# Kernel tuning notes

Hardware: AMD Instinct MI355X
Metric: run time of the kernel (lower is better)

## Reference

```python
import jax, jax.numpy as jnp
import numpy as np

NUM_HEADS = 8
IN_CH = 512
SCALING = float(IN_CH // 8) ** (-0.5)  # 0.125, as in the torch module


def _conv1x1(x, w, b):
    # x: [B,C,H,W], w: [O,C], b: [O]  (1x1 conv == channel matmul)
    return jnp.einsum('bchw,oc->bohw', x, w) + b[None, :, None, None]


def setup_inputs() -> dict:
    key = jax.random.key(0)
    ks = jax.random.split(key, 9)
    B, C, H, W = 4, IN_CH, 96, 96
    q = jax.random.normal(ks[0], (B, C, H, W), jnp.float32)
    v = jax.random.normal(ks[1], (B, C, H, W), jnp.float32)
    # xavier_uniform for [C,C] 1x1 conv weights
    limit = float(np.sqrt(6.0 / (C + C)))
    Wq = jax.random.uniform(ks[2], (C, C), jnp.float32, -limit, limit)
    Wk = jax.random.uniform(ks[3], (C, C), jnp.float32, -limit, limit)
    Wv = jax.random.uniform(ks[4], (C, C), jnp.float32, -limit, limit)
    bq = jnp.zeros((C,), jnp.float32)
    bk = jnp.zeros((C,), jnp.float32)
    bv = jnp.zeros((C,), jnp.float32)
    # gamma is init to 0 in the module; use a nonzero value so the output is nontrivial
    gamma = jax.random.normal(ks[5], (1,), jnp.float32) * 0.1
    return {'q': q, 'v': v, 'Wq': Wq, 'bq': bq, 'Wk': Wk, 'bk': bk,
            'Wv': Wv, 'bv': bv, 'gamma': gamma}


def reference(q, v, Wq, bq, Wk, bk, Wv, bv, gamma):
    B, C, H, W = q.shape
    nh = NUM_HEADS
    hd = C // nh
    t = _conv1x1(q, Wq, bq) * SCALING           # proj_query
    f = _conv1x1(q, Wk, bk)                     # proj_key
    g = _conv1x1(v, Wv, bv)                     # proj_value
    t = t.reshape(B * nh, hd, H, W)
    f = f.reshape(B * nh, hd, H, W)
    g = g.reshape(B * nh, hd, H, W)
    # criss-cross affinity: row (same y, all x') and column (same x, all y'!=y)
    e_row = jnp.einsum('bdyx,bdyi->byxi', t, f)  # [Bh, H, W, W]
    e_col = jnp.einsum('bdyx,bdix->byxi', t, f)  # [Bh, H, W, H]
    # exclude the current position from the column branch (CUDA kernel skips i==y)
    diag = (jnp.arange(H)[:, None, None] == jnp.arange(H)[None, None, :])  # [H,1,H]
    e_col = jnp.where(diag, -jnp.inf, e_col)
    attn = jax.nn.softmax(jnp.concatenate([e_row, e_col], axis=-1), axis=-1)  # [Bh,H,W,W+H]
    a_row, a_col = attn[..., :W], attn[..., W:]
    out = (jnp.einsum('byxi,bdyi->bdyx', a_row, g)
           + jnp.einsum('byxi,bdix->bdyx', a_col, g))  # [Bh, hd, H, W]
    out = out.reshape(B, C, H, W)
    return gamma[0] * out + v
```

## Files before the change

### kernel.cpp

```cpp
#include <hip/hip_runtime.h>
#include <hip/hip_bf16.h>

typedef __bf16 bf16;
typedef __attribute__((ext_vector_type(8))) __bf16 bf16x8;
typedef __attribute__((ext_vector_type(4))) float floatx4;

#define B_  4
#define C_  512
#define H_  96
#define W_  96
#define HD_ 64
#define HW_ 9216
#define BH_ 32
#define SCALING_ 0.125f
#define BHS_ 589824

static constexpr size_t T_ELEMS = (size_t)BH_ * HD_ * HW_;
static constexpr size_t S_ELEMS = (size_t)BH_ * HW_;

__global__ __launch_bounds__(256) void cast_w(
    const float* __restrict__ Wq, const float* __restrict__ Wk, const float* __restrict__ Wv,
    bf16* __restrict__ Wb)
{
    const int i  = blockIdx.x * 256 + threadIdx.x;
    const int e0 = i * 4;
    const int arr = e0 >> 18;
    const int off = e0 & 262143;
    const float* W = (arr == 0) ? Wq : (arr == 1) ? Wk : Wv;
    const float4 val = *(const float4*)(W + off);
    bf16 tmp[4] __attribute__((aligned(8)));
    tmp[0] = (bf16)val.x; tmp[1] = (bf16)val.y; tmp[2] = (bf16)val.z; tmp[3] = (bf16)val.w;
    *(uint2*)(Wb + e0) = *(const uint2*)tmp;
}

__global__ __launch_bounds__(256) void cast_qv(
    const float* __restrict__ q, const float* __restrict__ v,
    bf16* __restrict__ qbT, bf16* __restrict__ vbT)
{
    const int z = blockIdx.z;
    const int s = z >> 2, b = z & 3;
    const float* sb = (s ? v : q) + (size_t)b * C_ * HW_;
    bf16*       db = (s ? vbT : qbT) + (size_t)b * HW_ * C_;
    const int p0 = blockIdx.x * 64, c0 = blockIdx.y * 64;

    __shared__ float ts[64][65];
    const int tid = threadIdx.x;

    for (int i = tid; i < 1024; i += 256) {
        const int row = i >> 4, seg = i & 15;
        const float4 val = *(const float4*)(sb + (size_t)(c0 + row) * HW_ + p0 + seg * 4);
        ts[row][seg * 4 + 0] = val.x; ts[row][seg * 4 + 1] = val.y;
        ts[row][seg * 4 + 2] = val.z; ts[row][seg * 4 + 3] = val.w;
    }
    __syncthreads();
    for (int i = tid; i < 512; i += 256) {
        const int prow = i >> 3, cseg = i & 7;
        bf16 tmp[8] __attribute__((aligned(16)));
        #pragma unroll
        for (int k = 0; k < 8; k++) tmp[k] = (bf16)ts[cseg * 8 + k][prow];
        *(uint4*)(db + (size_t)(p0 + prow) * C_ + c0 + cseg * 8) = *(const uint4*)tmp;
    }
}

__device__ __forceinline__ void stage_tile(
    const bf16* __restrict__ A, const bf16* __restrict__ Bsrc,
    int o0, int p0, int k0, int tid, bf16* As, bf16* Bs)
{
    #pragma unroll
    for (int c = tid; c < 512; c += 256) {
        const int row = c >> 2, seg = c & 3;
        const bf16* gA = A    + (size_t)(o0 + row) * C_ + k0 + seg * 8;
        const bf16* gB = Bsrc + (size_t)(p0 + row) * C_ + k0 + seg * 8;
#if __has_builtin(__builtin_amdgcn_global_load_lds)
        char* lA = (char*)As + (size_t)(c & ~63) * 16;
        char* lB = (char*)Bs + (size_t)(c & ~63) * 16;
        __builtin_amdgcn_global_load_lds((const __attribute__((address_space(1))) void*)gA,
                                         (__attribute__((address_space(3))) void*)lA, 16, 0, 0);
        __builtin_amdgcn_global_load_lds((const __attribute__((address_space(1))) void*)gB,
                                         (__attribute__((address_space(3))) void*)lB, 16, 0, 0);
#else
        *(uint4*)((char*)As + (size_t)c * 16) = *(const uint4*)gA;
        *(uint4*)((char*)Bs + (size_t)c * 16) = *(const uint4*)gB;
#endif
    }
}

__device__ __forceinline__ void compute_tile(
    const bf16* As, const bf16* Bs,
    int mrow, int ncol, int l16, int quad, floatx4 acc[4][4])
{
    bf16x8 af[4], bf_[4];
    #pragma unroll
    for (int i = 0; i < 4; i++)
        af[i] = *(const bf16x8*)&As[(mrow + i * 16 + l16) * 32 + quad * 8];
    #pragma unroll
    for (int j = 0; j < 4; j++)
        bf_[j] = *(const bf16x8*)&Bs[(ncol + j * 16 + l16) * 32 + quad * 8];
    #pragma unroll
    for (int i = 0; i < 4; i++)
        #pragma unroll
        for (int j = 0; j < 4; j++)
            acc[i][j] = __builtin_amdgcn_mfma_f32_16x16x32_bf16(af[i], bf_[j], acc[i][j], 0, 0, 0);
}

__global__ __launch_bounds__(256) void conv_mfma(
    const bf16* __restrict__ Wb,
    const float* __restrict__ bq, const float* __restrict__ bk, const float* __restrict__ bv,
    const bf16* __restrict__ qbT, const bf16* __restrict__ vbT,
    bf16* __restrict__ tR, bf16* __restrict__ fR, bf16* __restrict__ g)
{
    const int z = blockIdx.z, arr = z >> 2, b = z & 3;
    const bf16* A    = Wb + (size_t)arr * C_ * C_;
    const bf16* Bsrc = ((arr == 2) ? vbT : qbT) + (size_t)b * HW_ * C_;
    const float* bias = (arr == 0) ? bq : (arr == 1) ? bk : bv;
    const float scale = (arr == 0) ? SCALING_ : 1.0f;

    const int p0 = blockIdx.x * 128;
    const int o0 = blockIdx.y * 128;

    __shared__ __align__(16) bf16 smem[17408];
    bf16* const As0 = smem;
    bf16* const Bs0 = smem + 4096;
    bf16* const As1 = smem + 8192;
    bf16* const Bs1 = smem + 12288;

    const int tid = threadIdx.x, lane = tid & 63;
    const int wave = tid >> 6, l16 = lane & 15, quad = lane >> 4;
    const int mrow = (wave >> 1) * 64, ncol = (wave & 1) * 64;

    floatx4 acc[4][4] = {};

    stage_tile(A, Bsrc, o0, p0, 0, tid, As0, Bs0);
    __syncthreads();

    for (int k0 = 0; k0 < C_; k0 += 64) {
        if (k0 + 32 < C_) stage_tile(A, Bsrc, o0, p0, k0 + 32, tid, As1, Bs1);
        compute_tile(As0, Bs0, mrow, ncol, l16, quad, acc);
        __syncthreads();
        if (k0 + 64 < C_) stage_tile(A, Bsrc, o0, p0, k0 + 64, tid, As0, Bs0);
        compute_tile(As1, Bs1, mrow, ncol, l16, quad, acc);
        __syncthreads();
    }

    const int TS = 136;
    if (arr < 2) {
        #pragma unroll
        for (int i = 0; i < 4; i++)
            #pragma unroll
            for (int r = 0; r < 4; r++) {
                const int ol_ = mrow + i * 16 + quad * 4 + r;
                const float bi = bias[o0 + ol_];
                #pragma unroll
                for (int j = 0; j < 4; j++) {
                    const int pl = ncol + j * 16 + l16;
                    smem[pl * TS + ol_] = (bf16)((acc[i][j][r] + bi) * scale);
                }
            }
        __syncthreads();
        bf16* dst = (arr == 0) ? tR : fR;
        #pragma unroll
        for (int c = tid; c < 2048; c += 256) {
            const int pl = c >> 4, oo = c & 15;
            const int pg = p0 + pl;
            const int y = pg / 96, x = pg - y * 96;
            const int og = o0 + oo * 8;
            const int bh = b * 8 + (og >> 6), d = og & 63;
            const size_t di = (size_t)bh * BHS_ + (size_t)y * 6144 + x * 64 + d;
            *(uint4*)(dst + di) = *(const uint4*)&smem[pl * TS + oo * 8];
        }
    } else {
        #pragma unroll
        for (int i = 0; i < 4; i++)
            #pragma unroll
            for (int r = 0; r < 4; r++) {
                const int ol_ = mrow + i * 16 + quad * 4 + r;
                const float bi = bias[o0 + ol_];
                #pragma unroll
                for (int j = 0; j < 4; j++) {
                    const int pl = ncol + j * 16 + l16;
                    smem[ol_ * TS + pl] = (bf16)(acc[i][j][r] + bi);
                }
            }
        __syncthreads();
        #pragma unroll
        for (int c = tid; c < 2048; c += 256) {
            const int ol_ = c >> 4, po = c & 15;
            const size_t di = (size_t)(b * 512 + o0 + ol_) * HW_ + p0 + po * 8;
            *(uint4*)(g + di) = *(const uint4*)&smem[ol_ * TS + po * 8];
        }
    }
}

__global__ __launch_bounds__(256) void transpose_g(const bf16* __restrict__ src, bf16* __restrict__ dst)
{
    const int plane = blockIdx.y;
    const int y0 = blockIdx.x * 32;
    const bf16* s = src + (size_t)plane * HW_;
    bf16*       d = dst + (size_t)plane * HW_;

    __shared__ bf16 ts[32][100];
    const int tid = threadIdx.x;

    #pragma unroll
    for (int i = tid; i < 768; i += 256) {
        const int row = i / 24, seg = i % 24;
        *(uint2*)&ts[row][seg * 4] = *(const uint2*)(s + (size_t)(y0 + row) * W_ + seg * 4);
    }
    __syncthreads();
    #pragma unroll
    for (int i = tid; i < 768; i += 256) {
        const int x = i >> 3, yseg = i & 7;
        bf16 tmp[4] __attribute__((aligned(8)));
        #pragma unroll
        for (int k = 0; k < 4; k++) tmp[k] = ts[yseg * 4 + k][x];
        *(uint2*)(d + (size_t)x * H_ + y0 + yseg * 4) = *(const uint2*)tmp;
    }
}

__global__ __launch_bounds__(512) void attn_col(
    const bf16* __restrict__ tR, const bf16* __restrict__ fR, const bf16* __restrict__ gT,
    bf16* __restrict__ outC, float* __restrict__ mc, float* __restrict__ lc)
{
    const int x = blockIdx.x;
    const int bh = blockIdx.y;

    __shared__ __align__(16) bf16 tl[96][72];
    __shared__ __align__(16) bf16 fl[96][72];
    __shared__ __align__(16) bf16 gl[64][104];
    __shared__ __align__(16) bf16 el[96][104];

    const int tid = threadIdx.x;
    const size_t sbase = (size_t)bh * BHS_;

    for (int i = tid; i < 768; i += 512) {
        const int y = i >> 3, oct = i & 7;
        const size_t gi = sbase + (size_t)y * 6144 + (size_t)x * 64 + oct * 8;
        *(uint4*)&tl[y][oct * 8] = *(const uint4*)(tR + gi);
        *(uint4*)&fl[y][oct * 8] = *(const uint4*)(fR + gi);
    }
    const size_t gbase = sbase + (size_t)x * 96;
    for (int i = tid; i < 768; i += 512) {
        const int d = i / 12, seg = i % 12;
        *(uint4*)&gl[d][seg * 8] = *(const uint4*)(gT + gbase + (size_t)d * HW_ + seg * 8);
    }
    __syncthreads();

    const int lane = tid & 63, wave = tid >> 6;
    const int l16 = lane & 15, quad = lane >> 4;

    #pragma unroll
    for (int it = 0; it < 5; it++) {
        const int idx = wave + it * 8;
        if (idx < 36) {
            const int mt = idx / 6, nt = idx % 6;
            floatx4 a = {};
            #pragma unroll
            for (int ks = 0; ks < 2; ks++) {
                bf16x8 af = *(const bf16x8*)&tl[mt * 16 + l16][ks * 32 + quad * 8];
                bf16x8 bf_ = *(const bf16x8*)&fl[nt * 16 + l16][ks * 32 + quad * 8];
                a = __builtin_amdgcn_mfma_f32_16x16x32_bf16(af, bf_, a, 0, 0, 0);
            }
            #pragma unroll
            for (int r = 0; r < 4; r++) {
                const int row = mt * 16 + quad * 4 + r, col = nt * 16 + l16;
                el[row][col] = (row == col) ? (bf16)(-1e30f) : (bf16)a[r];
            }
        }
    }
    __syncthreads();

    if (tid < 384) {
        const int r = tid >> 2, qu = tid & 3;
        float vals[24];
        float m = -1e30f;
        #pragma unroll
        for (int k = 0; k < 3; k++) {
            bf16x8 v8 = *(const bf16x8*)&el[r][qu * 24 + k * 8];
            #pragma unroll
            for (int e = 0; e < 8; e++) { vals[k * 8 + e] = (float)v8[e]; m = fmaxf(m, vals[k * 8 + e]); }
        }
        m = fmaxf(m, __shfl_xor(m, 1));
        m = fmaxf(m, __shfl_xor(m, 2));
        float s = 0.f;
        #pragma unroll
        for (int k = 0; k < 3; k++) {
            bf16 tmp[8] __attribute__((aligned(16)));
            #pragma unroll
            for (int e = 0; e < 8; e++) {
                const float p = __expf(vals[k * 8 + e] - m);
                s += p; tmp[e] = (bf16)p;
            }
            *(uint4*)&el[r][qu * 24 + k * 8] = *(const uint4*)tmp;
        }
        s += __shfl_xor(s, 1);
        s += __shfl_xor(s, 2);
        if (qu == 0) {
            mc[(size_t)bh * HW_ + x * 96 + r] = m;
            lc[(size_t)bh * HW_ + x * 96 + r] = s;
        }
    }
    __syncthreads();

    bf16 (*ol)[72] = tl;
    #pragma unroll
    for (int it = 0; it < 3; it++) {
        const int idx = wave + it * 8;
        const int mt = idx >> 2, nt = idx & 3;
        floatx4 a = {};
        #pragma unroll
        for (int ks = 0; ks < 3; ks++) {
            bf16x8 pf = *(const bf16x8*)&el[mt * 16 + l16][ks * 32 + quad * 8];
            bf16x8 gf = *(const bf16x8*)&gl[nt * 16 + l16][ks * 32 + quad * 8];
            a = __builtin_amdgcn_mfma_f32_16x16x32_bf16(pf, gf, a, 0, 0, 0);
        }
        #pragma unroll
        for (int r = 0; r < 4; r++)
            ol[mt * 16 + quad * 4 + r][nt * 16 + l16] = (bf16)a[r];
    }
    __syncthreads();

    bf16* ob = outC + sbase + (size_t)x * 6144;
    for (int i = tid; i < 768; i += 512) {
        const int j = i >> 3, oct = i & 7;
        *(uint4*)(ob + (size_t)j * 64 + oct * 8) = *(const uint4*)&ol[j][oct * 8];
    }
}

__global__ __launch_bounds__(512) void attn_row_merge(
    const bf16* __restrict__ tR, const bf16* __restrict__ fR, const bf16* __restrict__ g,
    const bf16* __restrict__ outC, const float* __restrict__ mc, const float* __restrict__ lc,
    const float* __restrict__ v, const float* __restrict__ gamma, float* __restrict__ out)
{
    const int y = blockIdx.x;
    const int bh = blockIdx.y;

    __shared__ __align__(16) bf16 tl[96][72];
    __shared__ __align__(16) bf16 fl[96][72];
    __shared__ __align__(16) bf16 gl[64][104];
    __shared__ __align__(16) bf16 el[96][104];
    __shared__ float mll[96], lll[96], wrl[96], wcl[96];

    const int tid = threadIdx.x;
    const size_t sbase = (size_t)bh * BHS_;
    const size_t slice = sbase + (size_t)y * 6144;

    for (int i = tid; i < 768; i += 512) {
        const int j = i >> 3, oct = i & 7;
        *(uint4*)&tl[j][oct * 8] = *(const uint4*)(tR + slice + (size_t)j * 64 + oct * 8);
        *(uint4*)&fl[j][oct * 8] = *(const uint4*)(fR + slice + (size_t)j * 64 + oct * 8);
    }
    const size_t gbase = sbase + (size_t)y * 96;
    for (int i = tid; i < 768; i += 512) {
        const int d = i / 12, seg = i % 12;
        *(uint4*)&gl[d][seg * 8] = *(const uint4*)(g + gbase + (size_t)d * HW_ + seg * 8);
    }
    __syncthreads();

    const int lane = tid & 63, wave = tid >> 6;
    const int l16 = lane & 15, quad = lane >> 4;

    #pragma unroll
    for (int it = 0; it < 5; it++) {
        const int idx = wave + it * 8;
        if (idx < 36) {
            const int mt = idx / 6, nt = idx % 6;
            floatx4 a = {};
            #pragma unroll
            for (int ks = 0; ks < 2; ks++) {
                bf16x8 af = *(const bf16x8*)&tl[mt * 16 + l16][ks * 32 + quad * 8];
                bf16x8 bf_ = *(const bf16x8*)&fl[nt * 16 + l16][ks * 32 + quad * 8];
                a = __builtin_amdgcn_mfma_f32_16x16x32_bf16(af, bf_, a, 0, 0, 0);
            }
            #pragma unroll
            for (int r = 0; r < 4; r++)
                el[mt * 16 + quad * 4 + r][nt * 16 + l16] = (bf16)a[r];
        }
    }
    __syncthreads();

    if (tid < 384) {
        const int r = tid >> 2, qu = tid & 3;
        float vals[24];
        float m = -1e30f;
        #pragma unroll
        for (int k = 0; k < 3; k++) {
            bf16x8 v8 = *(const bf16x8*)&el[r][qu * 24 + k * 8];
            #pragma unroll
            for (int e = 0; e < 8; e++) { vals[k * 8 + e] = (float)v8[e]; m = fmaxf(m, vals[k * 8 + e]); }
        }
        m = fmaxf(m, __shfl_xor(m, 1));
        m = fmaxf(m, __shfl_xor(m, 2));
        float s = 0.f;
        #pragma unroll
        for (int k = 0; k < 3; k++) {
            bf16 tmp[8] __attribute__((aligned(16)));
            #pragma unroll
            for (int e = 0; e < 8; e++) {
                const float p = __expf(vals[k * 8 + e] - m);
                s += p; tmp[e] = (bf16)p;
            }
            *(uint4*)&el[r][qu * 24 + k * 8] = *(const uint4*)tmp;
        }
        s += __shfl_xor(s, 1);
        s += __shfl_xor(s, 2);
        if (qu == 0) { mll[r] = m; lll[r] = s; }
    }
    __syncthreads();

    if (tid < 96) {
        const float mrv = mll[tid], lrv = lll[tid];
        const float mcv = mc[(size_t)bh * HW_ + tid * 96 + y];
        const float lcv = lc[(size_t)bh * HW_ + tid * 96 + y];
        const float mm = fmaxf(mrv, mcv);
        const float wr = __expf(mrv - mm), wc = __expf(mcv - mm);
        const float dn = lrv * wr + lcv * wc;
        wrl[tid] = wr / dn;
        wcl[tid] = wc / dn;
    }
    bf16 (*ocl)[72] = fl;
    for (int i = tid; i < 768; i += 512) {
        const int xx = i >> 3, oct = i & 7;
        *(uint4*)&ocl[xx][oct * 8] =
            *(const uint4*)(outC + sbase + (size_t)xx * 6144 + (size_t)y * 64 + oct * 8);
    }
    bf16 (*ol)[72] = tl;
    #pragma unroll
    for (int it = 0; it < 3; it++) {
        const int idx = wave + it * 8;
        const int mt = idx >> 2, nt = idx & 3;
        floatx4 a = {};
        #pragma unroll
        for (int ks = 0; ks < 3; ks++) {
            bf16x8 pf = *(const bf16x8*)&el[mt * 16 + l16][ks * 32 + quad * 8];
            bf16x8 gf = *(const bf16x8*)&gl[nt * 16 + l16][ks * 32 + quad * 8];
            a = __builtin_amdgcn_mfma_f32_16x16x32_bf16(pf, gf, a, 0, 0, 0);
        }
        #pragma unroll
        for (int r = 0; r < 4; r++)
            ol[mt * 16 + quad * 4 + r][nt * 16 + l16] = (bf16)a[r];
    }
    __syncthreads();

    const float gam = gamma[0];
    for (int i = tid; i < 768; i += 512) {
        const int xo = i >> 6, d = i & 63;
        const int x0 = xo * 8;
        float res[8];
        #pragma unroll
        for (int k = 0; k < 8; k++) {
            const int xx = x0 + k;
            res[k] = (float)ol[xx][d] * wrl[xx] + (float)ocl[xx][d] * wcl[xx];
        }
        const size_t ob = sbase + (size_t)d * HW_ + (size_t)y * 96 + x0;
        const float4 v0 = *(const float4*)(v + ob);
        const float4 v1 = *(const float4*)(v + ob + 4);
        float4 r0, r1;
        r0.x = gam * res[0] + v0.x; r0.y = gam * res[1] + v0.y;
        r0.z = gam * res[2] + v0.z; r0.w = gam * res[3] + v0.w;
        r1.x = gam * res[4] + v1.x; r1.y = gam * res[5] + v1.y;
        r1.z = gam * res[6] + v1.z; r1.w = gam * res[7] + v1.w;
        *(float4*)(out + ob) = r0;
        *(float4*)(out + ob + 4) = r1;
    }
}

extern "C" void kernel_launch(void* const* d_in, const int* in_sizes, int n_in,
                              void* d_out, int out_size, void* d_ws, size_t ws_size,
                              hipStream_t stream)
{
    const float* q     = (const float*)d_in[0];
    const float* v     = (const float*)d_in[1];
    const float* Wq    = (const float*)d_in[2];
    const float* bq    = (const float*)d_in[3];
    const float* Wk    = (const float*)d_in[4];
    const float* bk    = (const float*)d_in[5];
    const float* Wv    = (const float*)d_in[6];
    const float* bv    = (const float*)d_in[7];
    const float* gamma = (const float*)d_in[8];
    float* out = (float*)d_out;

    char* w = (char*)d_ws;
    const size_t Tb = T_ELEMS * sizeof(bf16);
    bf16* qbT  = (bf16*)(w + 0 * Tb);
    bf16* vbT  = (bf16*)(w + 1 * Tb);
    bf16* tR   = (bf16*)(w + 2 * Tb);
    bf16* fR   = (bf16*)(w + 3 * Tb);
    bf16* g    = (bf16*)(w + 4 * Tb);
    bf16* gT   = (bf16*)(w + 1 * Tb);
    bf16* outC = (bf16*)(w + 0 * Tb);
    bf16* Wb   = (bf16*)(w + 6 * Tb);
    float* mc  = (float*)(w + 6 * Tb + 1572864);
    float* lc  = mc + S_ELEMS;

    cast_w  <<<dim3(768), 256, 0, stream>>>(Wq, Wk, Wv, Wb);
    cast_qv <<<dim3(144, 8, 8), 256, 0, stream>>>(q, v, qbT, vbT);
    conv_mfma<<<dim3(72, 4, 12), 256, 0, stream>>>(Wb, bq, bk, bv, qbT, vbT, tR, fR, g);
    transpose_g<<<dim3(3, 2048), 256, 0, stream>>>(g, gT);
    attn_col<<<dim3(96, BH_), 512, 0, stream>>>(tR, fR, gT, outC, mc, lc);
    attn_row_merge<<<dim3(96, BH_), 512, 0, stream>>>(tR, fR, g, outC, mc, lc, v, gamma, out);
}
```

Before: 409.5 us.

## Fuse Q/K projections sharing input tile and swizzle LDS layouts

```diff
diff --git a/kernel.cpp b/kernel.cpp
--- a/kernel.cpp
+++ b/kernel.cpp
@@ -62,13 +62,14 @@
     }
 }
 
-__device__ __forceinline__ void stage_tile(
+__device__ __forceinline__ void stage_swz(
     const bf16* __restrict__ A, const bf16* __restrict__ Bsrc,
     int o0, int p0, int k0, int tid, bf16* As, bf16* Bs)
 {
     #pragma unroll
     for (int c = tid; c < 512; c += 256) {
-        const int row = c >> 2, seg = c & 3;
+        const int sc = c ^ ((c >> 3) & 7);
+        const int row = sc >> 2, seg = sc & 3;
         const bf16* gA = A    + (size_t)(o0 + row) * C_ + k0 + seg * 8;
         const bf16* gB = Bsrc + (size_t)(p0 + row) * C_ + k0 + seg * 8;
 #if __has_builtin(__builtin_amdgcn_global_load_lds)
@@ -85,17 +86,51 @@
     }
 }
 
-__device__ __forceinline__ void compute_tile(
+__device__ __forceinline__ void stage3_swz(
+    const bf16* __restrict__ A0, const bf16* __restrict__ A1, const bf16* __restrict__ Bsrc,
+    int o0, int p0, int k0, int tid, bf16* As0, bf16* As1, bf16* Bs)
+{
+    #pragma unroll
+    for (int c = tid; c < 512; c += 256) {
+        const int sc = c ^ ((c >> 3) & 7);
+        const int row = sc >> 2, seg = sc & 3;
+        const bf16* gA0 = A0   + (size_t)(o0 + row) * C_ + k0 + seg * 8;
+        const bf16* gA1 = A1   + (size_t)(o0 + row) * C_ + k0 + seg * 8;
+        const bf16* gB  = Bsrc + (size_t)(p0 + row) * C_ + k0 + seg * 8;
+#if __has_builtin(__builtin_amdgcn_global_load_lds)
+        char* lA0 = (char*)As0 + (size_t)(c & ~63) * 16;
+        char* lA1 = (char*)As1 + (size_t)(c & ~63) * 16;
+        char* lB  = (char*)Bs  + (size_t)(c & ~63) * 16;
+        __builtin_amdgcn_global_load_lds((const __attribute__((address_space(1))) void*)gA0,
+                                         (__attribute__((address_space(3))) void*)lA0, 16, 0, 0);
+        __builtin_amdgcn_global_load_lds((const __attribute__((address_space(1))) void*)gA1,
+                                         (__attribute__((address_space(3))) void*)lA1, 16, 0, 0);
+        __builtin_amdgcn_global_load_lds((const __attribute__((address_space(1))) void*)gB,
+                                         (__attribute__((address_space(3))) void*)lB, 16, 0, 0);
+#else
+        *(uint4*)((char*)As0 + (size_t)c * 16) = *(const uint4*)gA0;
+        *(uint4*)((char*)As1 + (size_t)c * 16) = *(const uint4*)gA1;
+        *(uint4*)((char*)Bs  + (size_t)c * 16) = *(const uint4*)gB;
+#endif
+    }
+}
+
+__device__ __forceinline__ int swz_chunk(int r, int quad)
+{
+    return (r * 4 + quad) ^ ((r >> 1) & 7);
+}
+
+__device__ __forceinline__ void compute_swz(
     const bf16* As, const bf16* Bs,
     int mrow, int ncol, int l16, int quad, floatx4 acc[4][4])
 {
     bf16x8 af[4], bf_[4];
     #pragma unroll
     for (int i = 0; i < 4; i++)
-        af[i] = *(const bf16x8*)&As[(mrow + i * 16 + l16) * 32 + quad * 8];
+        af[i] = *(const bf16x8*)&As[swz_chunk(mrow + i * 16 + l16, quad) * 8];
     #pragma unroll
     for (int j = 0; j < 4; j++)
-        bf_[j] = *(const bf16x8*)&Bs[(ncol + j * 16 + l16) * 32 + quad * 8];
+        bf_[j] = *(const bf16x8*)&Bs[swz_chunk(ncol + j * 16 + l16, quad) * 8];
     #pragma unroll
     for (int i = 0; i < 4; i++)
         #pragma unroll
@@ -103,47 +138,75 @@
             acc[i][j] = __builtin_amdgcn_mfma_f32_16x16x32_bf16(af[i], bf_[j], acc[i][j], 0, 0, 0);
 }
 
-__global__ __launch_bounds__(256) void conv_mfma(
+__device__ __forceinline__ void compute2_swz(
+    const bf16* As0, const bf16* As1, const bf16* Bs,
+    int mrow, int ncol, int l16, int quad, floatx4 acc0[4][4], floatx4 acc1[4][4])
+{
+    bf16x8 a0[4], a1[4], bb[4];
+    #pragma unroll
+    for (int i = 0; i < 4; i++) {
+        const int pc = swz_chunk(mrow + i * 16 + l16, quad);
+        a0[i] = *(const bf16x8*)&As0[pc * 8];
+        a1[i] = *(const bf16x8*)&As1[pc * 8];
+    }
+    #pragma unroll
+    for (int j = 0; j < 4; j++)
+        bb[j] = *(const bf16x8*)&Bs[swz_chunk(ncol + j * 16 + l16, quad) * 8];
+    #pragma unroll
+    for (int i = 0; i < 4; i++)
+        #pragma unroll
+        for (int j = 0; j < 4; j++)
+            acc0[i][j] = __builtin_amdgcn_mfma_f32_16x16x32_bf16(a0[i], bb[j], acc0[i][j], 0, 0, 0);
+    #pragma unroll
+    for (int i = 0; i < 4; i++)
+        #pragma unroll
+        for (int j = 0; j < 4; j++)
+            acc1[i][j] = __builtin_amdgcn_mfma_f32_16x16x32_bf16(a1[i], bb[j], acc1[i][j], 0, 0, 0);
+}
+
+__global__ __launch_bounds__(256, 2) void conv_qk(
     const bf16* __restrict__ Wb,
-    const float* __restrict__ bq, const float* __restrict__ bk, const float* __restrict__ bv,
-    const bf16* __restrict__ qbT, const bf16* __restrict__ vbT,
-    bf16* __restrict__ tR, bf16* __restrict__ fR, bf16* __restrict__ g)
-{
-    const int z = blockIdx.z, arr = z >> 2, b = z & 3;
-    const bf16* A    = Wb + (size_t)arr * C_ * C_;
-    const bf16* Bsrc = ((arr == 2) ? vbT : qbT) + (size_t)b * HW_ * C_;
-    const float* bias = (arr == 0) ? bq : (arr == 1) ? bk : bv;
-    const float scale = (arr == 0) ? SCALING_ : 1.0f;
+    const float* __restrict__ bq, const float* __restrict__ bk,
+    const bf16* __restrict__ qbT,
+    bf16* __restrict__ tR, bf16* __restrict__ fR)
+{
+    const int b = blockIdx.z;
+    const bf16* A0   = Wb;
+    const bf16* A1   = Wb + (size_t)C_ * C_;
+    const bf16* Bsrc = qbT + (size_t)b * HW_ * C_;
 
     const int p0 = blockIdx.x * 128;
     const int o0 = blockIdx.y * 128;
 
-    __shared__ __align__(16) bf16 smem[17408];
-    bf16* const As0 = smem;
-    bf16* const Bs0 = smem + 4096;
-    bf16* const As1 = smem + 8192;
-    bf16* const Bs1 = smem + 12288;
+    __shared__ __align__(16) bf16 smem[24576];
+    bf16* const As0_0 = smem;
+    bf16* const As1_0 = smem + 4096;
+    bf16* const Bs_0  = smem + 8192;
+    bf16* const As0_1 = smem + 12288;
+    bf16* const As1_1 = smem + 16384;
+    bf16* const Bs_1  = smem + 20480;
 
     const int tid = threadIdx.x, lane = tid & 63;
     const int wave = tid >> 6, l16 = lane & 15, quad = lane >> 4;
     const int mrow = (wave >> 1) * 64, ncol = (wave & 1) * 64;
 
-    floatx4 acc[4][4] = {};
-
-    stage_tile(A, Bsrc, o0, p0, 0, tid, As0, Bs0);
+    floatx4 acc0[4][4] = {};
+    floatx4 acc1[4][4] = {};
+
+    stage3_swz(A0, A1, Bsrc, o0, p0, 0, tid, As0_0, As1_0, Bs_0);
     __syncthreads();
 
     for (int k0 = 0; k0 < C_; k0 += 64) {
-        if (k0 + 32 < C_) stage_tile(A, Bsrc, o0, p0, k0 + 32, tid, As1, Bs1);
-        compute_tile(As0, Bs0, mrow, ncol, l16, quad, acc);
+        if (k0 + 32 < C_) stage3_swz(A0, A1, Bsrc, o0, p0, k0 + 32, tid, As0_1, As1_1, Bs_1);
+        compute2_swz(As0_0, As1_0, Bs_0, mrow, ncol, l16, quad, acc0, acc1);
         __syncthreads();
-        if (k0 + 64 < C_) stage_tile(A, Bsrc, o0, p0, k0 + 64, tid, As0, Bs0);
-        compute_tile(As1, Bs1, mrow, ncol, l16, quad, acc);
+        if (k0 + 64 < C_) stage3_swz(A0, A1, Bsrc, o0, p0, k0 + 64, tid, As0_0, As1_0, Bs_0);
+        compute2_swz(As0_1, As1_1, Bs_1, mrow, ncol, l16, quad, acc0, acc1);
         __syncthreads();
     }
 
-    const int TS = 136;
-    if (arr < 2) {
+    auto epi = [&](floatx4 (&ac)[4][4], const float* __restrict__ bias,
+                   float scale, bf16* __restrict__ dst) {
         #pragma unroll
         for (int i = 0; i < 4; i++)
             #pragma unroll
@@ -153,11 +216,10 @@
                 #pragma unroll
                 for (int j = 0; j < 4; j++) {
                     const int pl = ncol + j * 16 + l16;
-                    smem[pl * TS + ol_] = (bf16)((acc[i][j][r] + bi) * scale);
+                    smem[pl * 128 + (ol_ ^ ((pl & 7) << 3))] = (bf16)((ac[i][j][r] + bi) * scale);
                 }
             }
         __syncthreads();
-        bf16* dst = (arr == 0) ? tR : fR;
         #pragma unroll
         for (int c = tid; c < 2048; c += 256) {
             const int pl = c >> 4, oo = c & 15;
@@ -166,28 +228,70 @@
             const int og = o0 + oo * 8;
             const int bh = b * 8 + (og >> 6), d = og & 63;
             const size_t di = (size_t)bh * BHS_ + (size_t)y * 6144 + x * 64 + d;
-            *(uint4*)(dst + di) = *(const uint4*)&smem[pl * TS + oo * 8];
-        }
-    } else {
-        #pragma unroll
-        for (int i = 0; i < 4; i++)
-            #pragma unroll
-            for (int r = 0; r < 4; r++) {
-                const int ol_ = mrow + i * 16 + quad * 4 + r;
-                const float bi = bias[o0 + ol_];
-                #pragma unroll
-                for (int j = 0; j < 4; j++) {
-                    const int pl = ncol + j * 16 + l16;
-                    smem[ol_ * TS + pl] = (bf16)(acc[i][j][r] + bi);
-                }
+            *(uint4*)(dst + di) = *(const uint4*)&smem[pl * 128 + ((oo ^ (pl & 7)) * 8)];
+        }
+    };
+    epi(acc0, bq, SCALING_, tR);
+    __syncthreads();
+    epi(acc1, bk, 1.0f, fR);
+}
+
+__global__ __launch_bounds__(256) void conv_v(
+    const bf16* __restrict__ Wb,
+    const float* __restrict__ bv,
+    const bf16* __restrict__ vbT,
+    bf16* __restrict__ g)
+{
+    const int b = blockIdx.z;
+    const bf16* A    = Wb + (size_t)2 * C_ * C_;
+    const bf16* Bsrc = vbT + (size_t)b * HW_ * C_;
+
+    const int p0 = blockIdx.x * 128;
+    const int o0 = blockIdx.y * 128;
+
+    __shared__ __align__(16) bf16 smem[17408];
+    bf16* const As0 = smem;
+    bf16* const Bs0 = smem + 4096;
+    bf16* const As1 = smem + 8192;
+    bf16* const Bs1 = smem + 12288;
+
+    const int tid = threadIdx.x, lane = tid & 63;
+    const int wave = tid >> 6, l16 = lane & 15, quad = lane >> 4;
+    const int mrow = (wave >> 1) * 64, ncol = (wave & 1) * 64;
+
+    floatx4 acc[4][4] = {};
+
+    stage_swz(A, Bsrc, o0, p0, 0, tid, As0, Bs0);
+    __syncthreads();
+
+    for (int k0 = 0; k0 < C_; k0 += 64) {
+        if (k0 + 32 < C_) stage_swz(A, Bsrc, o0, p0, k0 + 32, tid, As1, Bs1);
+        compute_swz(As0, Bs0, mrow, ncol, l16, quad, acc);
+        __syncthreads();
+        if (k0 + 64 < C_) stage_swz(A, Bsrc, o0, p0, k0 + 64, tid, As0, Bs0);
+        compute_swz(As1, Bs1, mrow, ncol, l16, quad, acc);
+        __syncthreads();
+    }
+
+    const int TS = 136;
+    #pragma unroll
+    for (int i = 0; i < 4; i++)
+        #pragma unroll
+        for (int r = 0; r < 4; r++) {
+            const int ol_ = mrow + i * 16 + quad * 4 + r;
+            const float bi = bv[o0 + ol_];
+            #pragma unroll
+            for (int j = 0; j < 4; j++) {
+                const int pl = ncol + j * 16 + l16;
+                smem[ol_ * TS + pl] = (bf16)(acc[i][j][r] + bi);
             }
-        __syncthreads();
-        #pragma unroll
-        for (int c = tid; c < 2048; c += 256) {
-            const int ol_ = c >> 4, po = c & 15;
-            const size_t di = (size_t)(b * 512 + o0 + ol_) * HW_ + p0 + po * 8;
-            *(uint4*)(g + di) = *(const uint4*)&smem[ol_ * TS + po * 8];
-        }
+        }
+    __syncthreads();
+    #pragma unroll
+    for (int c = tid; c < 2048; c += 256) {
+        const int ol_ = c >> 4, po = c & 15;
+        const size_t di = (size_t)(b * 512 + o0 + ol_) * HW_ + p0 + po * 8;
+        *(uint4*)(g + di) = *(const uint4*)&smem[ol_ * TS + po * 8];
     }
 }
 
@@ -494,7 +598,8 @@
 
     cast_w  <<<dim3(768), 256, 0, stream>>>(Wq, Wk, Wv, Wb);
     cast_qv <<<dim3(144, 8, 8), 256, 0, stream>>>(q, v, qbT, vbT);
-    conv_mfma<<<dim3(72, 4, 12), 256, 0, stream>>>(Wb, bq, bk, bv, qbT, vbT, tR, fR, g);
+    conv_v  <<<dim3(72, 4, 4), 256, 0, stream>>>(Wb, bv, vbT, g);
+    conv_qk <<<dim3(72, 4, 4), 256, 0, stream>>>(Wb, bq, bk, qbT, tR, fR);
     transpose_g<<<dim3(3, 2048), 256, 0, stream>>>(g, gT);
     attn_col<<<dim3(96, BH_), 512, 0, stream>>>(tR, fR, gT, outC, mc, lc);
     attn_row_merge<<<dim3(96, BH_), 512, 0, stream>>>(tR, fR, g, outC, mc, lc, v, gamma, out);
```

After: 416.8 us. About the same (+1.8%).

## Swizzle conv GEMM LDS tiles and prefetch row-kernel epilogue loads early

Applied to the files above, without the earlier changes.

```diff
diff --git a/kernel.cpp b/kernel.cpp
--- a/kernel.cpp
+++ b/kernel.cpp
@@ -62,13 +62,14 @@
     }
 }
 
-__device__ __forceinline__ void stage_tile(
+__device__ __forceinline__ void stage_swz(
     const bf16* __restrict__ A, const bf16* __restrict__ Bsrc,
     int o0, int p0, int k0, int tid, bf16* As, bf16* Bs)
 {
     #pragma unroll
     for (int c = tid; c < 512; c += 256) {
-        const int row = c >> 2, seg = c & 3;
+        const int sc = c ^ ((c >> 3) & 7);
+        const int row = sc >> 2, seg = sc & 3;
         const bf16* gA = A    + (size_t)(o0 + row) * C_ + k0 + seg * 8;
         const bf16* gB = Bsrc + (size_t)(p0 + row) * C_ + k0 + seg * 8;
 #if __has_builtin(__builtin_amdgcn_global_load_lds)
@@ -85,17 +86,22 @@
     }
 }
 
-__device__ __forceinline__ void compute_tile(
+__device__ __forceinline__ int swz_chunk(int r, int quad)
+{
+    return (r * 4 + quad) ^ ((r >> 1) & 7);
+}
+
+__device__ __forceinline__ void compute_swz(
     const bf16* As, const bf16* Bs,
     int mrow, int ncol, int l16, int quad, floatx4 acc[4][4])
 {
     bf16x8 af[4], bf_[4];
     #pragma unroll
     for (int i = 0; i < 4; i++)
-        af[i] = *(const bf16x8*)&As[(mrow + i * 16 + l16) * 32 + quad * 8];
+        af[i] = *(const bf16x8*)&As[swz_chunk(mrow + i * 16 + l16, quad) * 8];
     #pragma unroll
     for (int j = 0; j < 4; j++)
-        bf_[j] = *(const bf16x8*)&Bs[(ncol + j * 16 + l16) * 32 + quad * 8];
+        bf_[j] = *(const bf16x8*)&Bs[swz_chunk(ncol + j * 16 + l16, quad) * 8];
     #pragma unroll
     for (int i = 0; i < 4; i++)
         #pragma unroll
@@ -130,19 +136,18 @@
 
     floatx4 acc[4][4] = {};
 
-    stage_tile(A, Bsrc, o0, p0, 0, tid, As0, Bs0);
+    stage_swz(A, Bsrc, o0, p0, 0, tid, As0, Bs0);
     __syncthreads();
 
     for (int k0 = 0; k0 < C_; k0 += 64) {
-        if (k0 + 32 < C_) stage_tile(A, Bsrc, o0, p0, k0 + 32, tid, As1, Bs1);
-        compute_tile(As0, Bs0, mrow, ncol, l16, quad, acc);
+        if (k0 + 32 < C_) stage_swz(A, Bsrc, o0, p0, k0 + 32, tid, As1, Bs1);
+        compute_swz(As0, Bs0, mrow, ncol, l16, quad, acc);
         __syncthreads();
-        if (k0 + 64 < C_) stage_tile(A, Bsrc, o0, p0, k0 + 64, tid, As0, Bs0);
-        compute_tile(As1, Bs1, mrow, ncol, l16, quad, acc);
+        if (k0 + 64 < C_) stage_swz(A, Bsrc, o0, p0, k0 + 64, tid, As0, Bs0);
+        compute_swz(As1, Bs1, mrow, ncol, l16, quad, acc);
         __syncthreads();
     }
 
-    const int TS = 136;
     if (arr < 2) {
         #pragma unroll
         for (int i = 0; i < 4; i++)
@@ -153,7 +158,7 @@
                 #pragma unroll
                 for (int j = 0; j < 4; j++) {
                     const int pl = ncol + j * 16 + l16;
-                    smem[pl * TS + ol_] = (bf16)((acc[i][j][r] + bi) * scale);
+                    smem[pl * 128 + (ol_ ^ ((pl & 7) << 3))] = (bf16)((acc[i][j][r] + bi) * scale);
                 }
             }
         __syncthreads();
@@ -166,9 +171,10 @@
             const int og = o0 + oo * 8;
             const int bh = b * 8 + (og >> 6), d = og & 63;
             const size_t di = (size_t)bh * BHS_ + (size_t)y * 6144 + x * 64 + d;
-            *(uint4*)(dst + di) = *(const uint4*)&smem[pl * TS + oo * 8];
+            *(uint4*)(dst + di) = *(const uint4*)&smem[pl * 128 + ((oo ^ (pl & 7)) * 8)];
         }
     } else {
+        const int TS = 136;
         #pragma unroll
         for (int i = 0; i < 4; i++)
             #pragma unroll
@@ -354,6 +360,34 @@
         const int d = i / 12, seg = i % 12;
         *(uint4*)&gl[d][seg * 8] = *(const uint4*)(g + gbase + (size_t)d * HW_ + seg * 8);
     }
+
+    uint4 oc0, oc1 = {};
+    {
+        const int xx = tid >> 3, oct = tid & 7;
+        oc0 = *(const uint4*)(outC + sbase + (size_t)xx * 6144 + (size_t)y * 64 + oct * 8);
+    }
+    if (tid < 256) {
+        const int i1 = tid + 512, xx = i1 >> 3, oct = i1 & 7;
+        oc1 = *(const uint4*)(outC + sbase + (size_t)xx * 6144 + (size_t)y * 64 + oct * 8);
+    }
+    float4 vp0a, vp0b, vp1a = {}, vp1b = {};
+    {
+        const int xo = tid >> 6, d = tid & 63;
+        const size_t ob = sbase + (size_t)d * HW_ + (size_t)y * 96 + xo * 8;
+        vp0a = *(const float4*)(v + ob);
+        vp0b = *(const float4*)(v + ob + 4);
+    }
+    if (tid < 256) {
+        const int i1 = tid + 512, xo = i1 >> 6, d = i1 & 63;
+        const size_t ob = sbase + (size_t)d * HW_ + (size_t)y * 96 + xo * 8;
+        vp1a = *(const float4*)(v + ob);
+        vp1b = *(const float4*)(v + ob + 4);
+    }
+    float mcv = 0.f, lcv = 0.f;
+    if (tid < 96) {
+        mcv = mc[(size_t)bh * HW_ + tid * 96 + y];
+        lcv = lc[(size_t)bh * HW_ + tid * 96 + y];
+    }
     __syncthreads();
 
     const int lane = tid & 63, wave = tid >> 6;
@@ -378,6 +412,16 @@
     }
     __syncthreads();
 
+    bf16 (*ocl)[72] = fl;
+    {
+        const int xx = tid >> 3, oct = tid & 7;
+        *(uint4*)&ocl[xx][oct * 8] = oc0;
+    }
+    if (tid < 256) {
+        const int i1 = tid + 512, xx = i1 >> 3, oct = i1 & 7;
+        *(uint4*)&ocl[xx][oct * 8] = oc1;
+    }
+
     if (tid < 384) {
         const int r = tid >> 2, qu = tid & 3;
         float vals[24];
@@ -409,20 +453,12 @@
 
     if (tid < 96) {
         const float mrv = mll[tid], lrv = lll[tid];
-        const float mcv = mc[(size_t)bh * HW_ + tid * 96 + y];
-        const float lcv = lc[(size_t)bh * HW_ + tid * 96 + y];
         const float mm = fmaxf(mrv, mcv);
         const float wr = __expf(mrv - mm), wc = __expf(mcv - mm);
         const float dn = lrv * wr + lcv * wc;
         wrl[tid] = wr / dn;
         wcl[tid] = wc / dn;
     }
-    bf16 (*ocl)[72] = fl;
-    for (int i = tid; i < 768; i += 512) {
-        const int xx = i >> 3, oct = i & 7;
-        *(uint4*)&ocl[xx][oct * 8] =
-            *(const uint4*)(outC + sbase + (size_t)xx * 6144 + (size_t)y * 64 + oct * 8);
-    }
     bf16 (*ol)[72] = tl;
     #pragma unroll
     for (int it = 0; it < 3; it++) {
@@ -442,8 +478,8 @@
     __syncthreads();
 
     const float gam = gamma[0];
-    for (int i = tid; i < 768; i += 512) {
-        const int xo = i >> 6, d = i & 63;
+    {
+        const int xo = tid >> 6, d = tid & 63;
         const int x0 = xo * 8;
         float res[8];
         #pragma unroll
@@ -452,13 +488,30 @@
             res[k] = (float)ol[xx][d] * wrl[xx] + (float)ocl[xx][d] * wcl[xx];
         }
         const size_t ob = sbase + (size_t)d * HW_ + (size_t)y * 96 + x0;
-        const float4 v0 = *(const float4*)(v + ob);
-        const float4 v1 = *(const float4*)(v + ob + 4);
         float4 r0, r1;
-        r0.x = gam * res[0] + v0.x; r0.y = gam * res[1] + v0.y;
-        r0.z = gam * res[2] + v0.z; r0.w = gam * res[3] + v0.w;
-        r1.x = gam * res[4] + v1.x; r1.y = gam * res[5] + v1.y;
-        r1.z = gam * res[6] + v1.z; r1.w = gam * res[7] + v1.w;
+        r0.x = gam * res[0] + vp0a.x; r0.y = gam * res[1] + vp0a.y;
+        r0.z = gam * res[2] + vp0a.z; r0.w = gam * res[3] + vp0a.w;
+        r1.x = gam * res[4] + vp0b.x; r1.y = gam * res[5] + vp0b.y;
+        r1.z = gam * res[6] + vp0b.z; r1.w = gam * res[7] + vp0b.w;
+        *(float4*)(out + ob) = r0;
+        *(float4*)(out + ob + 4) = r1;
+    }
+    if (tid < 256) {
+        const int i1 = tid + 512;
+        const int xo = i1 >> 6, d = i1 & 63;
+        const int x0 = xo * 8;
+        float res[8];
+        #pragma unroll
+        for (int k = 0; k < 8; k++) {
+            const int xx = x0 + k;
+            res[k] = (float)ol[xx][d] * wrl[xx] + (float)ocl[xx][d] * wcl[xx];
+        }
+        const size_t ob = sbase + (size_t)d * HW_ + (size_t)y * 96 + x0;
+        float4 r0, r1;
+        r0.x = gam * res[0] + vp1a.x; r0.y = gam * res[1] + vp1a.y;
+        r0.z = gam * res[2] + vp1a.z; r0.w = gam * res[3] + vp1a.w;
+        r1.x = gam * res[4] + vp1b.x; r1.y = gam * res[5] + vp1b.y;
+        r1.z = gam * res[6] + vp1b.z; r1.w = gam * res[7] + vp1b.w;
         *(float4*)(out + ob) = r0;
         *(float4*)(out + ob + 4) = r1;
     }
```

Result: faster. 400.6 us (-2.2%).
